# Optimization experiments

Measured on AMD Instinct MI355X. Metric: run time of the kernel, lower is better.

The kernel has to match this reference:

```python
import jax, jax.numpy as jnp
import numpy as np

H = 64           # edge/node/global hidden size
IN_F = 4         # node_attr_size
OUT_F = 1        # out_size
NUM_EMB = 100    # edge_num_embeddings
SKIP = True


def setup_inputs() -> dict:
    key = jax.random.key(0)
    ks = jax.random.split(key, 24)
    T, N, E = 4, 20000, 320000
    NNZ = 340000
    inp = {
        'node_attr': jax.random.normal(ks[0], (T, N, IN_F), jnp.float32),
        'global_attr': jax.random.normal(ks[1], (1, H), jnp.float32),
        'L_values': jax.random.normal(ks[2], (NNZ,), jnp.float32),
        'coeff': jnp.ones((1,), jnp.float32),
        'edge_attr': jax.random.randint(ks[3], (T, E), 0, NUM_EMB),
        'edge_index': jax.random.randint(ks[4], (2, E), 0, N),
        'L_index': jax.random.randint(ks[5], (2, NNZ), 0, N),
        'num_processing_steps': 4,
        # parameters
        'emb': jax.random.normal(ks[6], (NUM_EMB, H), jnp.float32) * 0.05,
        'W_ne': jax.random.normal(ks[7], (IN_F, H), jnp.float32) * 0.1,
        'b_ne': jnp.zeros((H,), jnp.float32),
        'W_eb': jax.random.normal(ks[8], ((H + 2 * H) * 2 + H, H), jnp.float32) * 0.05,
        'b_eb': jnp.zeros((H,), jnp.float32),
        'W_nb': jax.random.normal(ks[9], (2 * H + 2 * H + H, H), jnp.float32) * 0.05,
        'b_nb': jnp.zeros((H,), jnp.float32),
        'W_gb': jax.random.normal(ks[10], (H + H + H, H), jnp.float32) * 0.05,
        'b_gb': jnp.zeros((H,), jnp.float32),
        'W_d1': jax.random.normal(ks[11], (H, H), jnp.float32) * 0.1,
        'b_d1': jnp.zeros((H,), jnp.float32),
        'W_d2': jax.random.normal(ks[12], (H, OUT_F), jnp.float32) * 0.1,
        'b_d2': jnp.zeros((OUT_F,), jnp.float32),
        'W_i1': jax.random.normal(ks[13], (H, H), jnp.float32) * 0.1,
        'b_i1': jnp.zeros((H,), jnp.float32),
        'W_i2': jax.random.normal(ks[14], (H, IN_F), jnp.float32) * 0.1,
        'b_i2': jnp.zeros((IN_F,), jnp.float32),
    }
    return inp


def reference(node_attr, global_attr, L_values, coeff, emb, W_ne, b_ne,
              W_eb, b_eb, W_nb, b_nb, W_gb, b_gb, W_d1, b_d1, W_d2, b_d2,
              W_i1, b_i1, W_i2, b_i2, edge_attr, edge_index, L_index,
              num_processing_steps):
    T, N, _ = node_attr.shape
    s, r = edge_index[0], edge_index[1]
    Li, Lj = L_index[0], L_index[1]

    # encoders (all T steps at once)
    x_enc = jax.nn.relu(node_attr @ W_ne + b_ne)   # [T,N,H]
    e_enc = emb[edge_attr]                         # [T,E,H]

    def laplacian(h):  # sparse sp_L @ h, h: [N,H]
        return jax.ops.segment_sum(L_values[:, None] * h[Lj], Li, num_segments=N)

    def step(carry, xe):
        h_x, h_e, h_g = carry
        x_t, e_t = xe
        node_cat = jnp.concatenate([x_t, h_x], axis=-1)          # [N,2H]
        edge_cat = jnp.concatenate([e_t, h_e], axis=-1)          # [E,2H]
        g = h_g[0]                                               # [H]
        E_ = edge_cat.shape[0]
        # EdgeBlock: edges + sender + receiver + globals
        eb_in = jnp.concatenate([edge_cat, node_cat[s], node_cat[r],
                                 jnp.broadcast_to(g, (E_, g.shape[0]))], axis=-1)
        e_new = jax.nn.relu(eb_in @ W_eb + b_eb)                 # [E,H]
        # NodeBlock: scatter_add aggregates of received/sent edges
        recv = jax.ops.segment_sum(e_new, r, num_segments=N)
        sent = jax.ops.segment_sum(e_new, s, num_segments=N)
        nb_in = jnp.concatenate([recv, sent, node_cat,
                                 jnp.broadcast_to(g, (N, g.shape[0]))], axis=-1)
        x_new = jax.nn.relu(nb_in @ W_nb + b_nb)                 # [N,H]
        # GlobalBlock: scatter_mean (single graph -> mean)
        gb_in = jnp.concatenate([e_new.mean(0), x_new.mean(0), g])[None]
        g_new = jax.nn.relu(gb_in @ W_gb + b_gb)                 # [1,H]
        h_x_next = h_x + x_new if SKIP else x_new
        time_d = h_x_next - h_x
        spat_d = coeff[0] * laplacian(h_x_next)  # pde='diff': coeff * L u
        return (h_x_next, e_new, g_new), (h_x_next, time_d, spat_d)

    h0 = (jnp.zeros((N, H), jnp.float32),
          jnp.zeros((e_enc.shape[1], H), jnp.float32),
          global_attr)
    _, (hid, time_d, spat_d) = jax.lax.scan(step, h0, (x_enc, e_enc))

    # decoders over all steps
    out_nodes = jax.nn.relu(hid @ W_d1 + b_d1) @ W_d2 + b_d2     # [T,N,OUT_F]
    pred_in = jax.nn.relu(hid @ W_i1 + b_i1) @ W_i2 + b_i2       # [T,N,IN_F]
    return out_nodes, time_d, spat_d, pred_in
```

## Files before the change

### kernel.cpp

```cpp
#include <hip/hip_runtime.h>

#define TT 4
#define NN 20000
#define EE 320000
#define NZ 340000
#define NBKT 2500

typedef __attribute__((ext_vector_type(8))) __bf16 bf16x8;
typedef __attribute__((ext_vector_type(16))) float f32x16;

__device__ __forceinline__ unsigned short f2bf(float f) {
    unsigned int u = __float_as_uint(f);
    u = (u + 0x7FFFu + ((u >> 16) & 1u)) >> 16;
    return (unsigned short)u;
}
__device__ __forceinline__ float bf2f(unsigned short h) {
    return __uint_as_float(((unsigned int)h) << 16);
}

#define GLL16(src, dst) __builtin_amdgcn_global_load_lds( \
    (const __attribute__((address_space(1))) unsigned int*)(src), \
    (__attribute__((address_space(3))) unsigned int*)(dst), 16, 0, 0)

#define XB (TT * NN / 4)
#define CB ((NZ + 255) / 256)

__global__ __launch_bounds__(256) void k_setup(
    const float* __restrict__ na, const float* __restrict__ W_ne,
    const float* __restrict__ b_ne, unsigned short* __restrict__ xenc,
    const int* __restrict__ r, const int* __restrict__ s,
    const int* __restrict__ Li, int* cnt_r, int* cnt_s, int* cnt_L,
    const float* __restrict__ W_eb, const float* __restrict__ W_nb,
    const float* __restrict__ W_d1, const float* __restrict__ W_i1,
    const float* __restrict__ emb, unsigned short* __restrict__ Bpe,
    unsigned short* __restrict__ Bpu, unsigned short* __restrict__ Bpn,
    unsigned short* __restrict__ Bpd, unsigned short* __restrict__ emb_bf) {
    int bid = blockIdx.x;
    if (bid < XB) {
        int row = bid * 4 + (threadIdx.x >> 6);
        int j = threadIdx.x & 63;
        float4 a = *(const float4*)&na[(size_t)row * 4];
        float v = b_ne[j] + a.x * W_ne[j] + a.y * W_ne[64 + j] + a.z * W_ne[128 + j] + a.w * W_ne[192 + j];
        xenc[(size_t)row * 64 + j] = f2bf(fmaxf(v, 0.f));
        return;
    }
    bid -= XB;
    if (bid < CB) {
        int i = bid * 256 + threadIdx.x;
        if (i < EE) { atomicAdd(&cnt_r[r[i]], 1); atomicAdd(&cnt_s[s[i]], 1); }
        if (i < NZ) { atomicAdd(&cnt_L[Li[i]], 1); }
        return;
    }
    bid -= CB;
    int t = bid * 256 + threadIdx.x;
    if (t < 2 * 8 * 512) {
        int i = t & 7, l = (t >> 3) & 63, kb = (t >> 9) & 7, ch = t >> 12;
        int colv = ch * 32 + (l & 31);
        int k = kb * 16 + (l >> 5) * 8 + i;
        Bpe[t] = f2bf(W_eb[k * 64 + colv]);
    }
    if (t < 4 * 8 * 512) {
        int i = t & 7, l = (t >> 3) & 63, kb = (t >> 9) & 7, g = t >> 12;
        int colv = (g & 1) * 32 + (l & 31);
        int k = 128 + (g >> 1) * 128 + kb * 16 + (l >> 5) * 8 + i;
        Bpu[t] = f2bf(W_eb[k * 64 + colv]);
    }
    if (t < 2 * 16 * 512) {
        int i = t & 7, l = (t >> 3) & 63, kb = (t >> 9) % 16, ch = t / (16 * 512);
        int colv = ch * 32 + (l & 31);
        int k = kb * 16 + (l >> 5) * 8 + i;
        Bpn[t] = f2bf(W_nb[k * 64 + colv]);
    }
    if (t < 4 * 4 * 512) {
        int i = t & 7, l = (t >> 3) & 63, kb = (t >> 9) & 3, sec = t >> 11;
        int colv = (sec & 1) * 32 + (l & 31);
        int k = kb * 16 + (l >> 5) * 8 + i;
        const float* W = (sec < 2) ? W_d1 : W_i1;
        Bpd[t] = f2bf(W[k * 64 + colv]);
    }
    if (t < 100 * 64) emb_bf[t] = f2bf(emb[t]);
}

__global__ __launch_bounds__(1024) void k_scan(int* cnt, int* rowp, int* wp) {
    int which = blockIdx.x;
    int* c = cnt + which * NN;
    int* row = rowp + which * (NN + 1);
    int* w = wp + which * NN;
    __shared__ int ssum[1024];
    int tid = threadIdx.x;
    const int CH = (NN + 1023) / 1024;
    int base = tid * CH;
    int s = 0;
    for (int i = 0; i < CH; ++i) { int idx = base + i; s += (idx < NN) ? c[idx] : 0; }
    ssum[tid] = s;
    __syncthreads();
    for (int o = 1; o < 1024; o <<= 1) {
        int v = (tid >= o) ? ssum[tid - o] : 0;
        __syncthreads();
        ssum[tid] += v;
        __syncthreads();
    }
    int run = (tid > 0) ? ssum[tid - 1] : 0;
    for (int i = 0; i < CH; ++i) {
        int idx = base + i;
        if (idx < NN) { row[idx] = run; w[idx] = run; run += c[idx]; }
    }
    if (tid == 1023) row[NN] = ssum[1023];
}

__global__ __launch_bounds__(256) void k_scatter(
    const int* __restrict__ r, const int* __restrict__ s,
    const int* __restrict__ Li, const int* __restrict__ Lj,
    const float* __restrict__ Lv,
    int* wp_r, int* wp_s, int* wp_L,
    int* col_r, int* col_s, uint2* col_L8) {
    const int bucket = blockIdx.x & 7;
    const int nlo = bucket * NBKT;
    const int cid = blockIdx.x >> 3;
    const int stride = (gridDim.x >> 3) * 256;
    for (int i = cid * 256 + threadIdx.x; i < EE; i += stride) {
        int rv = r[i];
        if ((unsigned)(rv - nlo) < (unsigned)NBKT)
            col_r[atomicAdd(&wp_r[rv], 1)] = i;
        int sv = s[i];
        if ((unsigned)(sv - nlo) < (unsigned)NBKT)
            col_s[atomicAdd(&wp_s[sv], 1)] = i;
    }
    for (int i = cid * 256 + threadIdx.x; i < NZ; i += stride) {
        int lv = Li[i];
        if ((unsigned)(lv - nlo) < (unsigned)NBKT) {
            int pos = atomicAdd(&wp_L[lv], 1);
            uint2 v;
            v.x = (unsigned int)Lj[i];
            v.y = __float_as_uint(Lv[i]);
            col_L8[pos] = v;
        }
    }
}

__global__ __launch_bounds__(64) void k_usr(
    int do_update,
    const unsigned short* __restrict__ xenc_t, const unsigned short* __restrict__ hx_bf,
    const unsigned short* __restrict__ Bpu, unsigned int* __restrict__ usr,
    const float* __restrict__ W_gb, const float* __restrict__ b_gb,
    const float* __restrict__ W_eb, const float* __restrict__ b_eb,
    const float* __restrict__ W_nb, const float* __restrict__ b_nb,
    float* __restrict__ g_cur, float* __restrict__ e_sum, float* __restrict__ x_sum,
    float* __restrict__ gb_eb, float* __restrict__ gb_nb) {
    const int ln = threadIdx.x;
    const int er = ln & 31, hi = ln >> 5;

    if (blockIdx.x == 0) {
        int j = ln;
        float gv = g_cur[j];
        if (do_update) {
            float a = b_gb[j];
            for (int k = 0; k < 64; ++k) a += (e_sum[k] / (float)EE) * W_gb[k * 64 + j];
            for (int k = 0; k < 64; ++k) a += (x_sum[k] / (float)NN) * W_gb[(64 + k) * 64 + j];
            for (int k = 0; k < 64; ++k) a += g_cur[k] * W_gb[(128 + k) * 64 + j];
            gv = fmaxf(a, 0.f);
            g_cur[j] = gv;
            e_sum[j] = 0.f;
            x_sum[j] = 0.f;
        }
        float a1 = b_eb[j], a2 = b_nb[j];
        for (int k = 0; k < 64; ++k) {
            float gk = __shfl(gv, k, 64);
            a1 = fmaf(gk, W_eb[(384 + k) * 64 + j], a1);
            a2 = fmaf(gk, W_nb[(256 + k) * 64 + j], a2);
        }
        gb_eb[j] = a1;
        gb_nb[j] = a2;
    }

    const int n0 = blockIdx.x * 32;
    const int n = n0 + er;

    f32x16 a0, a1, a2, a3;
    #pragma unroll
    for (int i = 0; i < 16; ++i) { a0[i] = 0.f; a1[i] = 0.f; a2[i] = 0.f; a3[i] = 0.f; }

    const unsigned short* sx = xenc_t + (size_t)64 * n + hi * 8;
    const unsigned short* sh = hx_bf + (size_t)64 * n + hi * 8;
    #pragma unroll
    for (int c = 0; c < 2; ++c) {
        const unsigned short* src = c ? sh : sx;
        #pragma unroll
        for (int kb = 0; kb < 4; ++kb) {
            bf16x8 a = *(const bf16x8*)(src + kb * 16);
            int kg = c * 4 + kb;
            bf16x8 b0 = *(const bf16x8*)&Bpu[(size_t)((0 * 8 + kg) * 64 + ln) * 8];
            bf16x8 b1 = *(const bf16x8*)&Bpu[(size_t)((1 * 8 + kg) * 64 + ln) * 8];
            bf16x8 b2 = *(const bf16x8*)&Bpu[(size_t)((2 * 8 + kg) * 64 + ln) * 8];
            bf16x8 b3 = *(const bf16x8*)&Bpu[(size_t)((3 * 8 + kg) * 64 + ln) * 8];
            a0 = __builtin_amdgcn_mfma_f32_32x32x16_bf16(a, b0, a0, 0, 0, 0);
            a1 = __builtin_amdgcn_mfma_f32_32x32x16_bf16(a, b1, a1, 0, 0, 0);
            a2 = __builtin_amdgcn_mfma_f32_32x32x16_bf16(a, b2, a2, 0, 0, 0);
            a3 = __builtin_amdgcn_mfma_f32_32x32x16_bf16(a, b3, a3, 0, 0, 0);
        }
    }
    #pragma unroll
    for (int r = 0; r < 16; ++r) {
        int row = (r & 3) + 8 * (r >> 2) + 4 * hi;
        size_t o = (size_t)(n0 + row) * 64;
        usr[o + er]      = (unsigned int)f2bf(a0[r]) | ((unsigned int)f2bf(a1[r]) << 16);
        usr[o + 32 + er] = (unsigned int)f2bf(a2[r]) | ((unsigned int)f2bf(a3[r]) << 16);
    }
}

__global__ __launch_bounds__(512) void k_edge(
    int first, unsigned short* __restrict__ h_e,
    const unsigned short* __restrict__ emb_bf,
    const unsigned int* __restrict__ usr, const int* __restrict__ eattr_t,
    const int* __restrict__ sidx, const int* __restrict__ ridx,
    const unsigned short* __restrict__ Bp, const float* __restrict__ gbias,
    float* __restrict__ e_sum) {
    __shared__ unsigned short sBe[8192];
    __shared__ float sRed[8][64];
    const int tid = threadIdx.x;
    const int w = tid >> 6, ln = tid & 63;
    const int er = ln & 31, hi = ln >> 5;
    const int ebase = blockIdx.x * 256 + w * 32;
    const int e = ebase + er;

    const int siv = sidx[ebase + er];
    const int riv = ridx[ebase + er];
    const int ai = eattr_t[e];

    #pragma unroll
    for (int i = 0; i < 2; ++i) {
        int off = i * 4096 + w * 512;
        GLL16(Bp + off + ln * 8, sBe + off);
    }

    const unsigned short* s0 = emb_bf + (size_t)64 * ai + hi * 8;
    const unsigned short* s1 = h_e + (size_t)64 * e + hi * 8;
    bf16x8 a0 = *(const bf16x8*)(s0);
    bf16x8 a1 = *(const bf16x8*)(s0 + 16);
    bf16x8 a2 = *(const bf16x8*)(s0 + 32);
    bf16x8 a3 = *(const bf16x8*)(s0 + 48);
    bf16x8 a4{}, a5{}, a6{}, a7{};
    if (!first) {
        a4 = *(const bf16x8*)(s1);
        a5 = *(const bf16x8*)(s1 + 16);
        a6 = *(const bf16x8*)(s1 + 32);
        a7 = *(const bf16x8*)(s1 + 48);
    }

    f32x16 acc0, acc1;
    #pragma unroll
    for (int i = 0; i < 16; ++i) { acc0[i] = 0.f; acc1[i] = 0.f; }

    __syncthreads();

    #define EMM(AF, KG)                                                              \
        {                                                                            \
            bf16x8 b0 = *(const bf16x8*)&sBe[(((KG)) * 64 + ln) * 8];                \
            bf16x8 b1 = *(const bf16x8*)&sBe[((8 + (KG)) * 64 + ln) * 8];            \
            acc0 = __builtin_amdgcn_mfma_f32_32x32x16_bf16(AF, b0, acc0, 0, 0, 0);   \
            acc1 = __builtin_amdgcn_mfma_f32_32x32x16_bf16(AF, b1, acc1, 0, 0, 0);   \
        }
    EMM(a0, 0) EMM(a1, 1) EMM(a2, 2) EMM(a3, 3)
    if (!first) {
        EMM(a4, 4) EMM(a5, 5) EMM(a6, 6) EMM(a7, 7)
    }
    #undef EMM

    const float gb0 = gbias[er], gb1 = gbias[er + 32];
    float cs0 = 0.f, cs1 = 0.f;
    #pragma unroll
    for (int r = 0; r < 16; ++r) {
        int row = (r & 3) + 8 * (r >> 2) + 4 * hi;
        int si_row = __shfl(siv, row, 64);
        int ri_row = __shfl(riv, row, 64);
        unsigned int us = usr[(size_t)si_row * 64 + er];
        unsigned int ur = usr[(size_t)ri_row * 64 + 32 + er];
        size_t o = (size_t)(ebase + row) * 64;
        float v0 = fmaxf(acc0[r] + bf2f((unsigned short)(us & 0xFFFF))
                                 + bf2f((unsigned short)(ur & 0xFFFF)) + gb0, 0.f);
        float v1 = fmaxf(acc1[r] + bf2f((unsigned short)(us >> 16))
                                 + bf2f((unsigned short)(ur >> 16)) + gb1, 0.f);
        cs0 += v0; cs1 += v1;
        h_e[o + er] = f2bf(v0);
        h_e[o + er + 32] = f2bf(v1);
    }
    cs0 += __shfl_xor(cs0, 32, 64);
    cs1 += __shfl_xor(cs1, 32, 64);
    if (hi == 0) { sRed[w][er] = cs0; sRed[w][er + 32] = cs1; }
    __syncthreads();
    if (w == 0) {
        float t = 0.f;
        #pragma unroll
        for (int q = 0; q < 8; ++q) t += sRed[q][ln];
        atomicAdd(&e_sum[ln], t);
    }
}

__global__ __launch_bounds__(256) void k_glap(
    int gatherb,
    const unsigned short* __restrict__ h_e, const int* __restrict__ row_r,
    const int* __restrict__ col_r, const int* __restrict__ row_s,
    const int* __restrict__ col_s, unsigned short* __restrict__ recv,
    unsigned short* __restrict__ sentb,
    const unsigned short* __restrict__ hx_bf, const int* __restrict__ row_L,
    const uint2* __restrict__ col_L8, const float* __restrict__ coeff,
    float* __restrict__ spat_prev) {
    if ((int)blockIdx.x < gatherb) {
        int t = blockIdx.x * 256 + threadIdx.x;
        int sub = t & 31, n = t >> 5;
        int g = sub & 15, which = sub >> 4;
        const int* rowp = which ? row_s : row_r;
        const int* colp = which ? col_s : col_r;
        unsigned short* outp = which ? sentb : recv;

        float a0 = 0.f, a1 = 0.f, a2 = 0.f, a3 = 0.f;
        int b0 = rowp[n], b1 = rowp[n + 1];
        for (int p = b0; p < b1; ++p) {
            uint2 v = *(const uint2*)&h_e[(size_t)64 * colp[p] + g * 4];
            a0 += bf2f((unsigned short)(v.x & 0xFFFF));
            a1 += bf2f((unsigned short)(v.x >> 16));
            a2 += bf2f((unsigned short)(v.y & 0xFFFF));
            a3 += bf2f((unsigned short)(v.y >> 16));
        }
        uint2 packed;
        packed.x = (unsigned int)f2bf(a0) | ((unsigned int)f2bf(a1) << 16);
        packed.y = (unsigned int)f2bf(a2) | ((unsigned int)f2bf(a3) << 16);
        *(uint2*)&outp[(size_t)64 * n + g * 4] = packed;
        return;
    }
    int t = ((int)blockIdx.x - gatherb) * 256 + threadIdx.x;
    int sub = t & 31, n = t >> 5;
    int g = sub & 15, half = sub >> 4;
    float a0 = 0.f, a1 = 0.f, a2 = 0.f, a3 = 0.f;
    int b0 = row_L[n], b1 = row_L[n + 1];
    int mid = b0 + ((b1 - b0) >> 1);
    int p0 = half ? mid : b0;
    int p1 = half ? b1 : mid;
    for (int p = p0; p < p1; ++p) {
        uint2 e = col_L8[p];
        float lv = __uint_as_float(e.y);
        uint2 hv = *(const uint2*)&hx_bf[(size_t)64 * e.x + g * 4];
        a0 = fmaf(lv, bf2f((unsigned short)(hv.x & 0xFFFF)), a0);
        a1 = fmaf(lv, bf2f((unsigned short)(hv.x >> 16)), a1);
        a2 = fmaf(lv, bf2f((unsigned short)(hv.y & 0xFFFF)), a2);
        a3 = fmaf(lv, bf2f((unsigned short)(hv.y >> 16)), a3);
    }
    a0 += __shfl_xor(a0, 16, 64);
    a1 += __shfl_xor(a1, 16, 64);
    a2 += __shfl_xor(a2, 16, 64);
    a3 += __shfl_xor(a3, 16, 64);
    if (half == 0) {
        float c = coeff[0];
        float4 outv = {c * a0, c * a1, c * a2, c * a3};
        *(float4*)&spat_prev[(size_t)64 * n + g * 4] = outv;
    }
}

#define NODE_CHUNK(CIDX, BASE)                                                          \
    {                                                                                   \
        const unsigned short* src = (BASE) + hi * 8;                                    \
        _Pragma("unroll") for (int kb = 0; kb < 4; ++kb) {                              \
            bf16x8 a = *(const bf16x8*)(src + kb * 16);                                 \
            bf16x8 b0 = *(const bf16x8*)&Bp[(size_t)(((CIDX)*4 + kb) * 64 + ln) * 8];   \
            bf16x8 b1 = *(const bf16x8*)&Bp[(size_t)((16 + (CIDX)*4 + kb) * 64 + ln) * 8]; \
            acc0 = __builtin_amdgcn_mfma_f32_32x32x16_bf16(a, b0, acc0, 0, 0, 0);       \
            acc1 = __builtin_amdgcn_mfma_f32_32x32x16_bf16(a, b1, acc1, 0, 0, 0);       \
        }                                                                               \
    }

__global__ __launch_bounds__(64) void k_node(
    const unsigned short* __restrict__ recv, const unsigned short* __restrict__ sentb,
    const unsigned short* __restrict__ xenc_t, float* __restrict__ h_x,
    unsigned short* __restrict__ hx_bf, const unsigned short* __restrict__ Bp,
    const float* __restrict__ gbias, float* __restrict__ x_sum,
    unsigned short* __restrict__ hid_t, float* __restrict__ timed_t) {
    const int ln = threadIdx.x;
    const int er = ln & 31, hi = ln >> 5;
    const int n0 = blockIdx.x * 32;
    const int n = n0 + er;

    f32x16 acc0, acc1;
    #pragma unroll
    for (int i = 0; i < 16; ++i) { acc0[i] = 0.f; acc1[i] = 0.f; }

    NODE_CHUNK(0, recv + (size_t)64 * n)
    NODE_CHUNK(1, sentb + (size_t)64 * n)
    NODE_CHUNK(2, xenc_t + (size_t)64 * n)
    NODE_CHUNK(3, hx_bf + (size_t)64 * n)

    const float gb0 = gbias[er], gb1 = gbias[er + 32];
    float cs0 = 0.f, cs1 = 0.f;
    #pragma unroll
    for (int r = 0; r < 16; ++r) {
        int row = (r & 3) + 8 * (r >> 2) + 4 * hi;
        size_t o = (size_t)(n0 + row) * 64;
        float x0 = fmaxf(acc0[r] + gb0, 0.f);
        float x1 = fmaxf(acc1[r] + gb1, 0.f);
        cs0 += x0; cs1 += x1;
        float hx0 = h_x[o + er] + x0;
        float hx1 = h_x[o + er + 32] + x1;
        unsigned short hb0 = f2bf(hx0), hb1 = f2bf(hx1);
        h_x[o + er] = hx0;        h_x[o + er + 32] = hx1;
        hx_bf[o + er] = hb0;      hx_bf[o + er + 32] = hb1;
        hid_t[o + er] = hb0;      hid_t[o + er + 32] = hb1;
        timed_t[o + er] = x0;     timed_t[o + er + 32] = x1;
    }
    cs0 += __shfl_xor(cs0, 32, 64);
    cs1 += __shfl_xor(cs1, 32, 64);
    if (hi == 0) {
        atomicAdd(&x_sum[er], cs0);
        atomicAdd(&x_sum[er + 32], cs1);
    }
}

__global__ __launch_bounds__(256) void k_dec(
    const unsigned short* __restrict__ hid_bf, const unsigned short* __restrict__ Bpd,
    const float* __restrict__ b_d1, const float* __restrict__ W_d2,
    const float* __restrict__ b_d2, const float* __restrict__ b_i1,
    const float* __restrict__ W_i2, const float* __restrict__ b_i2,
    float* __restrict__ out_nodes, float* __restrict__ pred_in) {
    __shared__ unsigned short sDec[4][32 * 138];
    const int tid = threadIdx.x;
    const int w = tid >> 6, ln = tid & 63;
    const int er = ln & 31, hi = ln >> 5;
    const int row0 = (blockIdx.x * 4 + w) * 32;

    f32x16 ad0, ad1, ai0, ai1;
    #pragma unroll
    for (int i = 0; i < 16; ++i) { ad0[i] = 0.f; ad1[i] = 0.f; ai0[i] = 0.f; ai1[i] = 0.f; }

    const unsigned short* src = hid_bf + (size_t)(row0 + er) * 64 + hi * 8;
    #pragma unroll
    for (int kb = 0; kb < 4; ++kb) {
        bf16x8 a = *(const bf16x8*)(src + kb * 16);
        bf16x8 bd0 = *(const bf16x8*)&Bpd[((0 * 4 + kb) * 64 + ln) * 8];
        bf16x8 bd1 = *(const bf16x8*)&Bpd[((4 + kb) * 64 + ln) * 8];
        bf16x8 bi0 = *(const bf16x8*)&Bpd[((8 + kb) * 64 + ln) * 8];
        bf16x8 bi1 = *(const bf16x8*)&Bpd[((12 + kb) * 64 + ln) * 8];
        ad0 = __builtin_amdgcn_mfma_f32_32x32x16_bf16(a, bd0, ad0, 0, 0, 0);
        ad1 = __builtin_amdgcn_mfma_f32_32x32x16_bf16(a, bd1, ad1, 0, 0, 0);
        ai0 = __builtin_amdgcn_mfma_f32_32x32x16_bf16(a, bi0, ai0, 0, 0, 0);
        ai1 = __builtin_amdgcn_mfma_f32_32x32x16_bf16(a, bi1, ai1, 0, 0, 0);
    }

    const float bd0v = b_d1[er], bd1v = b_d1[er + 32];
    const float bi0v = b_i1[er], bi1v = b_i1[er + 32];
    unsigned short* sw = &sDec[w][0];
    #pragma unroll
    for (int r = 0; r < 16; ++r) {
        int row = (r & 3) + 8 * (r >> 2) + 4 * hi;
        sw[row * 138 + er]       = f2bf(fmaxf(ad0[r] + bd0v, 0.f));
        sw[row * 138 + er + 32]  = f2bf(fmaxf(ad1[r] + bd1v, 0.f));
        sw[row * 138 + er + 64]  = f2bf(fmaxf(ai0[r] + bi0v, 0.f));
        sw[row * 138 + er + 96]  = f2bf(fmaxf(ai1[r] + bi1v, 0.f));
    }
    __syncthreads();

    const int g_row = row0 + er;
    if (hi == 0) {
        float s = 0.f;
        for (int k = 0; k < 32; ++k) {
            unsigned int u = *(const unsigned int*)&sw[er * 138 + 2 * k];
            s = fmaf(bf2f((unsigned short)(u & 0xFFFF)), W_d2[2 * k], s);
            s = fmaf(bf2f((unsigned short)(u >> 16)), W_d2[2 * k + 1], s);
        }
        out_nodes[g_row] = s + b_d2[0];
    } else {
        float s0 = 0.f, s1 = 0.f, s2 = 0.f, s3 = 0.f;
        for (int k = 0; k < 32; ++k) {
            unsigned int u = *(const unsigned int*)&sw[er * 138 + 64 + 2 * k];
            float vlo = bf2f((unsigned short)(u & 0xFFFF));
            float vhi = bf2f((unsigned short)(u >> 16));
            float4 w0 = *(const float4*)&W_i2[(2 * k) * 4];
            float4 w1 = *(const float4*)&W_i2[(2 * k + 1) * 4];
            s0 = fmaf(vlo, w0.x, fmaf(vhi, w1.x, s0));
            s1 = fmaf(vlo, w0.y, fmaf(vhi, w1.y, s1));
            s2 = fmaf(vlo, w0.z, fmaf(vhi, w1.z, s2));
            s3 = fmaf(vlo, w0.w, fmaf(vhi, w1.w, s3));
        }
        float4 pv = {s0 + b_i2[0], s1 + b_i2[1], s2 + b_i2[2], s3 + b_i2[3]};
        *(float4*)&pred_in[(size_t)4 * g_row] = pv;
    }
}

extern "C" void kernel_launch(void* const* d_in, const int* in_sizes, int n_in,
                              void* d_out, int out_size, void* d_ws, size_t ws_size,
                              hipStream_t stream) {
    (void)in_sizes; (void)n_in; (void)out_size; (void)ws_size;
    const float* node_attr   = (const float*)d_in[0];
    const float* global_attr = (const float*)d_in[1];
    const float* L_values    = (const float*)d_in[2];
    const float* coeff       = (const float*)d_in[3];
    const int*   edge_attr   = (const int*)d_in[4];
    const int*   edge_index  = (const int*)d_in[5];
    const int*   L_index     = (const int*)d_in[6];
    const float* emb  = (const float*)d_in[8];
    const float* W_ne = (const float*)d_in[9];
    const float* b_ne = (const float*)d_in[10];
    const float* W_eb = (const float*)d_in[11];
    const float* b_eb = (const float*)d_in[12];
    const float* W_nb = (const float*)d_in[13];
    const float* b_nb = (const float*)d_in[14];
    const float* W_gb = (const float*)d_in[15];
    const float* b_gb = (const float*)d_in[16];
    const float* W_d1 = (const float*)d_in[17];
    const float* b_d1 = (const float*)d_in[18];
    const float* W_d2 = (const float*)d_in[19];
    const float* b_d2 = (const float*)d_in[20];
    const float* W_i1 = (const float*)d_in[21];
    const float* b_i1 = (const float*)d_in[22];
    const float* W_i2 = (const float*)d_in[23];
    const float* b_i2 = (const float*)d_in[24];

    const int* s_idx = edge_index;
    const int* r_idx = edge_index + EE;
    const int* Li = L_index;
    const int* Lj = L_index + NZ;

    char* ws = (char*)d_ws;
    size_t off = 0;
    auto alloc = [&](size_t bytes) -> void* {
        void* p = ws + off;
        off = (off + bytes + 255) & ~(size_t)255;
        return p;
    };
    unsigned short* xenc   = (unsigned short*)alloc((size_t)TT * NN * 64 * 2);
    unsigned short* hid    = (unsigned short*)alloc((size_t)TT * NN * 64 * 2);
    float*          h_x    = (float*)alloc((size_t)NN * 64 * 4);
    unsigned short* hx_bf  = (unsigned short*)alloc((size_t)NN * 64 * 2);
    unsigned short* h_e    = (unsigned short*)alloc((size_t)EE * 64 * 2);
    unsigned short* recv   = (unsigned short*)alloc((size_t)NN * 64 * 2);
    unsigned short* sentb  = (unsigned short*)alloc((size_t)NN * 64 * 2);
    unsigned int*   usr    = (unsigned int*)alloc((size_t)NN * 64 * 4);
    float* smalls          = (float*)alloc(2048);
    unsigned short* Bpe    = (unsigned short*)alloc((size_t)2 * 8 * 512 * 2);
    unsigned short* Bpu    = (unsigned short*)alloc((size_t)4 * 8 * 512 * 2);
    unsigned short* Bpn    = (unsigned short*)alloc((size_t)2 * 16 * 512 * 2);
    unsigned short* Bpd    = (unsigned short*)alloc((size_t)4 * 4 * 512 * 2);
    unsigned short* emb_bf = (unsigned short*)alloc((size_t)100 * 64 * 2);
    int* cnt    = (int*)alloc((size_t)3 * NN * 4);
    int* rowp   = (int*)alloc((size_t)3 * (NN + 1) * 4);
    int* wp     = (int*)alloc((size_t)3 * NN * 4);
    int* col_r  = (int*)alloc((size_t)EE * 4);
    int* col_s  = (int*)alloc((size_t)EE * 4);
    uint2* col_L8 = (uint2*)alloc((size_t)NZ * 8);

    float* g_cur = smalls;
    float* e_sum = smalls + 64;
    float* x_sum = smalls + 128;
    float* gb_eb = smalls + 192;
    float* gb_nb = smalls + 256;
    int* cnt_r = cnt, *cnt_s = cnt + NN, *cnt_L = cnt + 2 * NN;
    int* row_r = rowp, *row_s = rowp + (NN + 1), *row_L = rowp + 2 * (NN + 1);
    int* wp_r = wp, *wp_s = wp + NN, *wp_L = wp + 2 * NN;

    float* out_nodes = (float*)d_out;
    float* time_d = out_nodes + (size_t)TT * NN;
    float* spat_d = time_d + (size_t)TT * NN * 64;
    float* pred_in = spat_d + (size_t)TT * NN * 64;

    hipMemsetAsync(h_x, 0, (size_t)NN * 64 * 4, stream);
    hipMemsetAsync(hx_bf, 0, (size_t)NN * 64 * 2, stream);
    hipMemsetAsync(smalls, 0, 2048, stream);
    hipMemsetAsync(cnt, 0, (size_t)3 * NN * 4, stream);
    hipMemcpyAsync(g_cur, global_attr, 64 * 4, hipMemcpyDeviceToDevice, stream);

    k_setup<<<XB + CB + 96, 256, 0, stream>>>(node_attr, W_ne, b_ne, xenc,
                                              r_idx, s_idx, Li, cnt_r, cnt_s, cnt_L,
                                              W_eb, W_nb, W_d1, W_i1, emb,
                                              Bpe, Bpu, Bpn, Bpd, emb_bf);
    k_scan<<<3, 1024, 0, stream>>>(cnt, rowp, wp);
    k_scatter<<<2048, 256, 0, stream>>>(r_idx, s_idx, Li, Lj, L_values,
                                        wp_r, wp_s, wp_L, col_r, col_s, col_L8);

    const int GB = NN * 32 / 256;
    for (int t = 0; t < TT; ++t) {
        const unsigned short* xenc_t = xenc + (size_t)t * NN * 64;
        k_usr<<<NN / 32, 64, 0, stream>>>(t > 0, xenc_t, hx_bf, Bpu, usr,
                                          W_gb, b_gb, W_eb, b_eb, W_nb, b_nb,
                                          g_cur, e_sum, x_sum, gb_eb, gb_nb);
        k_edge<<<EE / 256, 512, 0, stream>>>(t == 0, h_e, emb_bf, usr,
                                             edge_attr + (size_t)t * EE, s_idx, r_idx,
                                             Bpe, gb_eb, e_sum);
        int grid = GB + ((t > 0) ? GB : 0);
        float* spat_prev = spat_d + (size_t)((t > 0) ? t - 1 : 0) * NN * 64;
        k_glap<<<grid, 256, 0, stream>>>(GB, h_e, row_r, col_r, row_s, col_s,
                                         recv, sentb, hx_bf, row_L, col_L8, coeff,
                                         spat_prev);
        k_node<<<NN / 32, 64, 0, stream>>>(recv, sentb, xenc_t, h_x, hx_bf,
                                           Bpn, gb_nb, x_sum,
                                           hid + (size_t)t * NN * 64,
                                           time_d + (size_t)t * NN * 64);
    }
    k_glap<<<GB, 256, 0, stream>>>(0, h_e, row_r, col_r, row_s, col_s,
                                   recv, sentb, hx_bf, row_L, col_L8, coeff,
                                   spat_d + (size_t)(TT - 1) * NN * 64);
    k_dec<<<TT * NN / 128, 256, 0, stream>>>(hid, Bpd, b_d1, W_d2, b_d2,
                                             b_i1, W_i2, b_i2, out_nodes, pred_in);
}
```

Measured before the change: 634.3 us.

## Fold CSR scan and scatter into first-step usr and edge kernels

Removes the separate k_scan and k_scatter launches. The prefix scan now runs as 3 extra 64-thread blocks inside the first k_usr launch using wave shuffles, and the CSR scatter runs as extra blocks prepended to the first k_edge launch. The aim is to cut launch overhead and let this setup work overlap with the step-0 usr and edge compute. The risks are a single-wave scan that is serial over about 313 elements per lane, and 512-thread scatter blocks sharing k_edge's large LDS footprint, which could limit occupancy.

```diff
diff --git a/kernel.cpp b/kernel.cpp
--- a/kernel.cpp
+++ b/kernel.cpp
@@ -5,6 +5,7 @@
 #define EE 320000
 #define NZ 340000
 #define NBKT 2500
+#define SCB 2048
 
 typedef __attribute__((ext_vector_type(8))) __bf16 bf16x8;
 typedef __attribute__((ext_vector_type(16))) float f32x16;
@@ -36,15 +37,6 @@
     unsigned short* __restrict__ Bpu, unsigned short* __restrict__ Bpn,
     unsigned short* __restrict__ Bpd, unsigned short* __restrict__ emb_bf) {
     int bid = blockIdx.x;
-    if (bid < XB) {
-        int row = bid * 4 + (threadIdx.x >> 6);
-        int j = threadIdx.x & 63;
-        float4 a = *(const float4*)&na[(size_t)row * 4];
-        float v = b_ne[j] + a.x * W_ne[j] + a.y * W_ne[64 + j] + a.z * W_ne[128 + j] + a.w * W_ne[192 + j];
-        xenc[(size_t)row * 64 + j] = f2bf(fmaxf(v, 0.f));
-        return;
-    }
-    bid -= XB;
     if (bid < CB) {
         int i = bid * 256 + threadIdx.x;
         if (i < EE) { atomicAdd(&cnt_r[r[i]], 1); atomicAdd(&cnt_s[s[i]], 1); }
@@ -52,102 +44,79 @@
         return;
     }
     bid -= CB;
-    int t = bid * 256 + threadIdx.x;
-    if (t < 2 * 8 * 512) {
-        int i = t & 7, l = (t >> 3) & 63, kb = (t >> 9) & 7, ch = t >> 12;
-        int colv = ch * 32 + (l & 31);
-        int k = kb * 16 + (l >> 5) * 8 + i;
-        Bpe[t] = f2bf(W_eb[k * 64 + colv]);
-    }
-    if (t < 4 * 8 * 512) {
-        int i = t & 7, l = (t >> 3) & 63, kb = (t >> 9) & 7, g = t >> 12;
-        int colv = (g & 1) * 32 + (l & 31);
-        int k = 128 + (g >> 1) * 128 + kb * 16 + (l >> 5) * 8 + i;
-        Bpu[t] = f2bf(W_eb[k * 64 + colv]);
-    }
-    if (t < 2 * 16 * 512) {
-        int i = t & 7, l = (t >> 3) & 63, kb = (t >> 9) % 16, ch = t / (16 * 512);
-        int colv = ch * 32 + (l & 31);
-        int k = kb * 16 + (l >> 5) * 8 + i;
-        Bpn[t] = f2bf(W_nb[k * 64 + colv]);
-    }
-    if (t < 4 * 4 * 512) {
-        int i = t & 7, l = (t >> 3) & 63, kb = (t >> 9) & 3, sec = t >> 11;
-        int colv = (sec & 1) * 32 + (l & 31);
-        int k = kb * 16 + (l >> 5) * 8 + i;
-        const float* W = (sec < 2) ? W_d1 : W_i1;
-        Bpd[t] = f2bf(W[k * 64 + colv]);
-    }
-    if (t < 100 * 64) emb_bf[t] = f2bf(emb[t]);
-}
-
-__global__ __launch_bounds__(1024) void k_scan(int* cnt, int* rowp, int* wp) {
-    int which = blockIdx.x;
-    int* c = cnt + which * NN;
-    int* row = rowp + which * (NN + 1);
-    int* w = wp + which * NN;
-    __shared__ int ssum[1024];
-    int tid = threadIdx.x;
-    const int CH = (NN + 1023) / 1024;
-    int base = tid * CH;
-    int s = 0;
-    for (int i = 0; i < CH; ++i) { int idx = base + i; s += (idx < NN) ? c[idx] : 0; }
-    ssum[tid] = s;
-    __syncthreads();
-    for (int o = 1; o < 1024; o <<= 1) {
-        int v = (tid >= o) ? ssum[tid - o] : 0;
-        __syncthreads();
-        ssum[tid] += v;
-        __syncthreads();
-    }
-    int run = (tid > 0) ? ssum[tid - 1] : 0;
-    for (int i = 0; i < CH; ++i) {
-        int idx = base + i;
-        if (idx < NN) { row[idx] = run; w[idx] = run; run += c[idx]; }
-    }
-    if (tid == 1023) row[NN] = ssum[1023];
-}
-
-__global__ __launch_bounds__(256) void k_scatter(
-    const int* __restrict__ r, const int* __restrict__ s,
-    const int* __restrict__ Li, const int* __restrict__ Lj,
-    const float* __restrict__ Lv,
-    int* wp_r, int* wp_s, int* wp_L,
-    int* col_r, int* col_s, uint2* col_L8) {
-    const int bucket = blockIdx.x & 7;
-    const int nlo = bucket * NBKT;
-    const int cid = blockIdx.x >> 3;
-    const int stride = (gridDim.x >> 3) * 256;
-    for (int i = cid * 256 + threadIdx.x; i < EE; i += stride) {
-        int rv = r[i];
-        if ((unsigned)(rv - nlo) < (unsigned)NBKT)
-            col_r[atomicAdd(&wp_r[rv], 1)] = i;
-        int sv = s[i];
-        if ((unsigned)(sv - nlo) < (unsigned)NBKT)
-            col_s[atomicAdd(&wp_s[sv], 1)] = i;
-    }
-    for (int i = cid * 256 + threadIdx.x; i < NZ; i += stride) {
-        int lv = Li[i];
-        if ((unsigned)(lv - nlo) < (unsigned)NBKT) {
-            int pos = atomicAdd(&wp_L[lv], 1);
-            uint2 v;
-            v.x = (unsigned int)Lj[i];
-            v.y = __float_as_uint(Lv[i]);
-            col_L8[pos] = v;
-        }
-    }
+    if (bid < 96) {
+        int t = bid * 256 + threadIdx.x;
+        if (t < 2 * 8 * 512) {
+            int i = t & 7, l = (t >> 3) & 63, kb = (t >> 9) & 7, ch = t >> 12;
+            int colv = ch * 32 + (l & 31);
+            int k = kb * 16 + (l >> 5) * 8 + i;
+            Bpe[t] = f2bf(W_eb[k * 64 + colv]);
+        }
+        if (t < 4 * 8 * 512) {
+            int i = t & 7, l = (t >> 3) & 63, kb = (t >> 9) & 7, g = t >> 12;
+            int colv = (g & 1) * 32 + (l & 31);
+            int k = 128 + (g >> 1) * 128 + kb * 16 + (l >> 5) * 8 + i;
+            Bpu[t] = f2bf(W_eb[k * 64 + colv]);
+        }
+        if (t < 2 * 16 * 512) {
+            int i = t & 7, l = (t >> 3) & 63, kb = (t >> 9) % 16, ch = t / (16 * 512);
+            int colv = ch * 32 + (l & 31);
+            int k = kb * 16 + (l >> 5) * 8 + i;
+            Bpn[t] = f2bf(W_nb[k * 64 + colv]);
+        }
+        if (t < 4 * 4 * 512) {
+            int i = t & 7, l = (t >> 3) & 63, kb = (t >> 9) & 3, sec = t >> 11;
+            int colv = (sec & 1) * 32 + (l & 31);
+            int k = kb * 16 + (l >> 5) * 8 + i;
+            const float* W = (sec < 2) ? W_d1 : W_i1;
+            Bpd[t] = f2bf(W[k * 64 + colv]);
+        }
+        if (t < 100 * 64) emb_bf[t] = f2bf(emb[t]);
+        return;
+    }
+    bid -= 96;
+    int row = bid * 4 + (threadIdx.x >> 6);
+    int j = threadIdx.x & 63;
+    float4 a = *(const float4*)&na[(size_t)row * 4];
+    float v = b_ne[j] + a.x * W_ne[j] + a.y * W_ne[64 + j] + a.z * W_ne[128 + j] + a.w * W_ne[192 + j];
+    xenc[(size_t)row * 64 + j] = f2bf(fmaxf(v, 0.f));
 }
 
 __global__ __launch_bounds__(64) void k_usr(
-    int do_update,
+    int do_update, int nusr,
     const unsigned short* __restrict__ xenc_t, const unsigned short* __restrict__ hx_bf,
     const unsigned short* __restrict__ Bpu, unsigned int* __restrict__ usr,
     const float* __restrict__ W_gb, const float* __restrict__ b_gb,
     const float* __restrict__ W_eb, const float* __restrict__ b_eb,
     const float* __restrict__ W_nb, const float* __restrict__ b_nb,
     float* __restrict__ g_cur, float* __restrict__ e_sum, float* __restrict__ x_sum,
-    float* __restrict__ gb_eb, float* __restrict__ gb_nb) {
+    float* __restrict__ gb_eb, float* __restrict__ gb_nb,
+    int* __restrict__ cnt, int* __restrict__ rowp, int* __restrict__ wp) {
     const int ln = threadIdx.x;
+
+    if ((int)blockIdx.x >= nusr) {
+        int which = blockIdx.x - nusr;
+        int* c = cnt + which * NN;
+        int* row = rowp + which * (NN + 1);
+        int* w = wp + which * NN;
+        const int CHS = (NN + 63) / 64;
+        int base = ln * CHS;
+        int msum = 0;
+        for (int i = 0; i < CHS; ++i) { int idx = base + i; msum += (idx < NN) ? c[idx] : 0; }
+        int inc = msum;
+        for (int o = 1; o < 64; o <<= 1) {
+            int v = __shfl_up(inc, o, 64);
+            if (ln >= o) inc += v;
+        }
+        int run = inc - msum;
+        for (int i = 0; i < CHS; ++i) {
+            int idx = base + i;
+            if (idx < NN) { row[idx] = run; w[idx] = run; run += c[idx]; }
+        }
+        if (ln == 63) row[NN] = inc;
+        return;
+    }
+
     const int er = ln & 31, hi = ln >> 5;
 
     if (blockIdx.x == 0) {
@@ -209,18 +178,50 @@
 }
 
 __global__ __launch_bounds__(512) void k_edge(
-    int first, unsigned short* __restrict__ h_e,
+    int first, int scatterb, unsigned short* __restrict__ h_e,
     const unsigned short* __restrict__ emb_bf,
     const unsigned int* __restrict__ usr, const int* __restrict__ eattr_t,
     const int* __restrict__ sidx, const int* __restrict__ ridx,
     const unsigned short* __restrict__ Bp, const float* __restrict__ gbias,
-    float* __restrict__ e_sum) {
+    float* __restrict__ e_sum,
+    const int* __restrict__ Li, const int* __restrict__ Lj,
+    const float* __restrict__ Lv,
+    int* wp_r, int* wp_s, int* wp_L,
+    int* col_r, int* col_s, uint2* col_L8) {
     __shared__ unsigned short sBe[8192];
     __shared__ float sRed[8][64];
     const int tid = threadIdx.x;
+
+    if ((int)blockIdx.x < scatterb) {
+        const int sbid = blockIdx.x;
+        const int bucket = sbid & 7;
+        const int nlo = bucket * NBKT;
+        const int cid = sbid >> 3;
+        const int stride = (scatterb >> 3) * 512;
+        for (int i = cid * 512 + tid; i < EE; i += stride) {
+            int rv = ridx[i];
+            if ((unsigned)(rv - nlo) < (unsigned)NBKT)
+                col_r[atomicAdd(&wp_r[rv], 1)] = i;
+            int sv = sidx[i];
+            if ((unsigned)(sv - nlo) < (unsigned)NBKT)
+                col_s[atomicAdd(&wp_s[sv], 1)] = i;
+        }
+        for (int i = cid * 512 + tid; i < NZ; i += stride) {
+            int lv = Li[i];
+            if ((unsigned)(lv - nlo) < (unsigned)NBKT) {
+                int pos = atomicAdd(&wp_L[lv], 1);
+                uint2 v;
+                v.x = (unsigned int)Lj[i];
+                v.y = __float_as_uint(Lv[i]);
+                col_L8[pos] = v;
+            }
+        }
+        return;
+    }
+
     const int w = tid >> 6, ln = tid & 63;
     const int er = ln & 31, hi = ln >> 5;
-    const int ebase = blockIdx.x * 256 + w * 32;
+    const int ebase = ((int)blockIdx.x - scatterb) * 256 + w * 32;
     const int e = ebase + er;
 
     const int siv = sidx[ebase + er];
@@ -565,23 +566,24 @@
     hipMemsetAsync(cnt, 0, (size_t)3 * NN * 4, stream);
     hipMemcpyAsync(g_cur, global_attr, 64 * 4, hipMemcpyDeviceToDevice, stream);
 
-    k_setup<<<XB + CB + 96, 256, 0, stream>>>(node_attr, W_ne, b_ne, xenc,
+    k_setup<<<CB + 96 + XB, 256, 0, stream>>>(node_attr, W_ne, b_ne, xenc,
                                               r_idx, s_idx, Li, cnt_r, cnt_s, cnt_L,
                                               W_eb, W_nb, W_d1, W_i1, emb,
                                               Bpe, Bpu, Bpn, Bpd, emb_bf);
-    k_scan<<<3, 1024, 0, stream>>>(cnt, rowp, wp);
-    k_scatter<<<2048, 256, 0, stream>>>(r_idx, s_idx, Li, Lj, L_values,
-                                        wp_r, wp_s, wp_L, col_r, col_s, col_L8);
-
+
+    const int NUSR = NN / 32;
     const int GB = NN * 32 / 256;
     for (int t = 0; t < TT; ++t) {
         const unsigned short* xenc_t = xenc + (size_t)t * NN * 64;
-        k_usr<<<NN / 32, 64, 0, stream>>>(t > 0, xenc_t, hx_bf, Bpu, usr,
-                                          W_gb, b_gb, W_eb, b_eb, W_nb, b_nb,
-                                          g_cur, e_sum, x_sum, gb_eb, gb_nb);
-        k_edge<<<EE / 256, 512, 0, stream>>>(t == 0, h_e, emb_bf, usr,
-                                             edge_attr + (size_t)t * EE, s_idx, r_idx,
-                                             Bpe, gb_eb, e_sum);
+        k_usr<<<NUSR + ((t == 0) ? 3 : 0), 64, 0, stream>>>(
+            t > 0, NUSR, xenc_t, hx_bf, Bpu, usr,
+            W_gb, b_gb, W_eb, b_eb, W_nb, b_nb,
+            g_cur, e_sum, x_sum, gb_eb, gb_nb, cnt, rowp, wp);
+        int scb = (t == 0) ? SCB : 0;
+        k_edge<<<scb + EE / 256, 512, 0, stream>>>(
+            t == 0, scb, h_e, emb_bf, usr,
+            edge_attr + (size_t)t * EE, s_idx, r_idx, Bpe, gb_eb, e_sum,
+            Li, Lj, L_values, wp_r, wp_s, wp_L, col_r, col_s, col_L8);
         int grid = GB + ((t > 0) ? GB : 0);
         float* spat_prev = spat_d + (size_t)((t > 0) ? t - 1 : 0) * NN * 64;
         k_glap<<<grid, 256, 0, stream>>>(GB, h_e, row_r, col_r, row_s, col_s,
```

Result: slower. 660.6 us (+4.2%).
